# Optimization experiments

Hardware: AMD Instinct MI355X
Metric: run time of the kernel (lower is better)

Reference implementation:

```python
import jax, jax.numpy as jnp
import numpy as np

B, S, I, H = 16, 2048, 1024, 1024


def setup_inputs() -> dict:
    key = jax.random.key(0)
    ks = jax.random.split(key, 12)
    sc = 0.03  # small init so tanh/sigmoid are not saturated
    return {
        "x": jax.random.normal(ks[0], (B, S, I), dtype=jnp.float32),
        "attn_w1": sc * jax.random.normal(ks[1], (H, I), dtype=jnp.float32),
        "attn_b1": sc * jax.random.normal(ks[2], (H,), dtype=jnp.float32),
        "attn_w2": sc * jax.random.normal(ks[3], (1, H), dtype=jnp.float32),
        "attn_b2": sc * jax.random.normal(ks[4], (1,), dtype=jnp.float32),
        "w_ih": sc * jax.random.normal(ks[5], (3 * H, I), dtype=jnp.float32),
        "w_hh": sc * jax.random.normal(ks[6], (3 * H, H), dtype=jnp.float32),
        "b_ih": sc * jax.random.normal(ks[7], (3 * H,), dtype=jnp.float32),
        "b_hh": sc * jax.random.normal(ks[8], (3 * H,), dtype=jnp.float32),
        "fc_w": sc * jax.random.normal(ks[9], (I, H), dtype=jnp.float32),
        "fc_b": sc * jax.random.normal(ks[10], (I,), dtype=jnp.float32),
    }


def reference(x, attn_w1, attn_b1, attn_w2, attn_b2, w_ih, w_hh, b_ih, b_hh, fc_w, fc_b):
    b, s, i = x.shape
    h_dim = w_hh.shape[1]
    # Attention: per-timestep Linear-Tanh-Linear-Softmax, vectorized over time.
    ha = jnp.tanh(jnp.einsum('bsi,hi->bsh', x, attn_w1) + attn_b1)
    scores = jnp.einsum('bsh,oh->bso', ha, attn_w2) + attn_b2  # [B,S,1]
    # torch applies Softmax(dim=1) on [B,1] per timestep -> softmax over size-1 axis
    attn = jax.nn.softmax(scores, axis=2)  # [B,S,1] (identically ones)
    x_w = x * attn
    # GRU (1 layer): precompute input projections over all timesteps.
    gi = jnp.einsum('bsi,gi->bsg', x_w, w_ih) + b_ih  # [B,S,3H]

    def step(h, gi_t):
        gh = h @ w_hh.T + b_hh
        i_r, i_z, i_n = jnp.split(gi_t, 3, axis=-1)
        h_r, h_z, h_n = jnp.split(gh, 3, axis=-1)
        r = jax.nn.sigmoid(i_r + h_r)
        z = jax.nn.sigmoid(i_z + h_z)
        n = jnp.tanh(i_n + r * h_n)
        h_new = (1.0 - z) * n + z * h
        return h_new, h_new

    h0 = jnp.zeros((b, h_dim), dtype=x.dtype)
    h_last, outs = jax.lax.scan(step, h0, jnp.swapaxes(gi, 0, 1))  # outs: [S,B,H]
    rnn_out = jnp.swapaxes(outs, 0, 1)  # [B,S,H]
    output = jnp.einsum('bsh,ih->bsi', rnn_out, fc_w) + fc_b
    hidden = h_last[None]  # [num_layers=1, B, H]
    return (output, hidden, attn)
```

## Files before the change

### kernel.cpp

```cpp
#include <hip/hip_runtime.h>

typedef __attribute__((ext_vector_type(8))) short bh8;
typedef __attribute__((ext_vector_type(4))) float f32x4;

#define BATCH 16
#define SEQ 2048
#define M_ROWS (BATCH * SEQ)
#define KDIM 1024

__device__ __forceinline__ unsigned short f2bf(float f) {
  unsigned u = __float_as_uint(f);
  u = (u + 0x7FFFu + ((u >> 16) & 1u)) >> 16;
  return (unsigned short)u;
}
__device__ __forceinline__ float bf2f(unsigned short h) {
  return __uint_as_float(((unsigned)h) << 16);
}

__device__ __forceinline__ f32x4 mfma_bf16(bh8 a, bh8 b, f32x4 c) {
  return __builtin_amdgcn_mfma_f32_16x16x32_bf16(a, b, c, 0, 0, 0);
}

__device__ __forceinline__ void gl2lds16(const void* g, void* l) {
  __builtin_amdgcn_global_load_lds(
      (const __attribute__((address_space(1))) void*)g,
      (__attribute__((address_space(3))) void*)l, 16, 0, 0);
}

__global__ void cvt_bf16_kernel(const float* __restrict__ in,
                                unsigned short* __restrict__ out, int n4) {
  int i = blockIdx.x * blockDim.x + threadIdx.x;
  if (i >= n4) return;
  float4 v = ((const float4*)in)[i];
  ushort4 o;
  o.x = f2bf(v.x); o.y = f2bf(v.y); o.z = f2bf(v.z); o.w = f2bf(v.w);
  ((ushort4*)out)[i] = o;
}

__global__ void fill_ones_kernel(float* __restrict__ p, int n) {
  int i = blockIdx.x * blockDim.x + threadIdx.x;
  if (i < n) p[i] = 1.0f;
}

template<int MODE>
__global__ __launch_bounds__(256, 2) void gemm_nt(
    const unsigned short* __restrict__ A,
    const unsigned short* __restrict__ Bm,
    void* __restrict__ Cout,
    const float* __restrict__ bias,
    int N)
{
  __shared__ unsigned short As[128 * 32];
  __shared__ unsigned short Bs[128 * 32];
  const int tid = threadIdx.x;
  const int wave = tid >> 6, lane = tid & 63;
  const long tileM = (long)blockIdx.y * 128;
  const long tileN = (long)blockIdx.x * 128;

  const int srow = wave * 16 + (lane >> 2);
  const int scol = (lane & 3) * 8;
  const unsigned short* ga = A + (tileM + srow) * KDIM + scol;
  const unsigned short* gb = Bm + (tileN + srow) * KDIM + scol;
  unsigned short* la = As + wave * 512;
  unsigned short* lb = Bs + wave * 512;

  f32x4 acc[4][4];
  #pragma unroll
  for (int i = 0; i < 4; ++i)
    #pragma unroll
    for (int j = 0; j < 4; ++j)
      acc[i][j] = (f32x4){0.f, 0.f, 0.f, 0.f};

  const int wm = wave >> 1, wn = wave & 1;
  const int q = lane >> 4, mr = lane & 15;

  #pragma unroll 1
  for (int kt = 0; kt < 32; ++kt) {
    const int ko = kt * 32;
    gl2lds16(ga + ko, la);
    gl2lds16(ga + (long)64 * KDIM + ko, la + 2048);
    gl2lds16(gb + ko, lb);
    gl2lds16(gb + (long)64 * KDIM + ko, lb + 2048);
    __syncthreads();

    bh8 af[4], bfv[4];
    #pragma unroll
    for (int t = 0; t < 4; ++t)
      af[t] = *(const bh8*)&As[(wm * 64 + t * 16 + mr) * 32 + q * 8];
    #pragma unroll
    for (int t = 0; t < 4; ++t)
      bfv[t] = *(const bh8*)&Bs[(wn * 64 + t * 16 + mr) * 32 + q * 8];

    #pragma unroll
    for (int mt = 0; mt < 4; ++mt)
      #pragma unroll
      for (int nt = 0; nt < 4; ++nt)
        acc[mt][nt] = mfma_bf16(af[mt], bfv[nt], acc[mt][nt]);
    __syncthreads();
  }

  #pragma unroll
  for (int mt = 0; mt < 4; ++mt) {
    #pragma unroll
    for (int nt = 0; nt < 4; ++nt) {
      long n = tileN + wn * 64 + nt * 16 + mr;
      #pragma unroll
      for (int i = 0; i < 4; ++i) {
        long m = tileM + wm * 64 + mt * 16 + q * 4 + i;
        if constexpr (MODE == 0) {
          ((float*)Cout)[m * N + n] = acc[mt][nt][i] + bias[n];
        } else {
          int b = (int)(m >> 11), s = (int)(m & 2047);
          int g = (int)(n >> 10), wgi = (int)((n >> 4) & 63), dd = (int)(n & 15);
          size_t idx = ((size_t)s * 64 + wgi) * 768 + (size_t)g * 256 + b * 16 + dd;
          ((unsigned short*)Cout)[idx] = f2bf(acc[mt][nt][i]);
        }
      }
    }
  }
}

#define GRU_WGS 64
__global__ __launch_bounds__(256, 1) void gru_kernel(
    const unsigned short* __restrict__ gi,
    const unsigned short* __restrict__ whh,
    const float* __restrict__ b_ih,
    const float* __restrict__ b_hh,
    unsigned* __restrict__ hdw,
    unsigned* __restrict__ flags,
    unsigned short* __restrict__ rnn,
    float* __restrict__ hidden_out)
{
  const int wg = blockIdx.x;
  const int tid = threadIdx.x;
  const int wv = tid >> 6, lane = tid & 63;
  const int D0 = wg * 16;
  const int q = lane >> 4, nn = lane & 15;

  bh8 wf[3][8];
  #pragma unroll
  for (int g = 0; g < 3; ++g)
    #pragma unroll
    for (int kk = 0; kk < 8; ++kk) {
      int k = wv * 256 + kk * 32 + q * 8;
      wf[g][kk] = *(const bh8*)&whh[(size_t)(g * 1024 + D0 + nn) * 1024 + k];
    }

  const int b = tid >> 4, dd = tid & 15, d = D0 + dd;
  const float bir = b_ih[d], biz = b_ih[1024 + d], bin_ = b_ih[2048 + d];
  const float bhr = b_hh[d], bhz = b_hh[1024 + d], bhn = b_hh[2048 + d];
  float hreg = 0.0f;

  __shared__ float red[4][3][16][16];

  const unsigned short* g0 = gi + (size_t)wg * 768 + b * 16 + dd;
  unsigned short pg0 = g0[0], pg1 = g0[256], pg2 = g0[512];

  #pragma unroll 1
  for (int s = 0; s < SEQ; ++s) {
    float gir = bf2f(pg0), giz = bf2f(pg1), gin = bf2f(pg2);

    const unsigned* hrow = hdw + (s & 1) * 8192 + nn * 512 + wv * 128 + q * 4;
    unsigned t[32];
    #pragma unroll
    for (int kk = 0; kk < 8; ++kk)
      #pragma unroll
      for (int j = 0; j < 4; ++j)
        t[kk * 4 + j] = __hip_atomic_load(&hrow[kk * 16 + j], __ATOMIC_RELAXED,
                                          __HIP_MEMORY_SCOPE_AGENT);

    f32x4 acc0 = {0.f,0.f,0.f,0.f}, acc1 = {0.f,0.f,0.f,0.f}, acc2 = {0.f,0.f,0.f,0.f};
    #pragma unroll
    for (int kk = 0; kk < 8; ++kk) {
      union { unsigned w[4]; bh8 v; } u;
      u.w[0] = t[kk*4+0]; u.w[1] = t[kk*4+1]; u.w[2] = t[kk*4+2]; u.w[3] = t[kk*4+3];
      acc0 = mfma_bf16(u.v, wf[0][kk], acc0);
      acc1 = mfma_bf16(u.v, wf[1][kk], acc1);
      acc2 = mfma_bf16(u.v, wf[2][kk], acc2);
    }
    #pragma unroll
    for (int i = 0; i < 4; ++i) {
      red[wv][0][q * 4 + i][nn] = acc0[i];
      red[wv][1][q * 4 + i][nn] = acc1[i];
      red[wv][2][q * 4 + i][nn] = acc2[i];
    }
    __syncthreads();

    float ghr = red[0][0][b][dd] + red[1][0][b][dd] + red[2][0][b][dd] + red[3][0][b][dd];
    float ghz = red[0][1][b][dd] + red[1][1][b][dd] + red[2][1][b][dd] + red[3][1][b][dd];
    float ghn = red[0][2][b][dd] + red[1][2][b][dd] + red[2][2][b][dd] + red[3][2][b][dd];

    float xr = gir + bir + ghr + bhr;
    float xz = giz + biz + ghz + bhz;
    float r = 1.0f / (1.0f + __expf(-xr));
    float z = 1.0f / (1.0f + __expf(-xz));
    float u_ = gin + bin_ + r * (ghn + bhn);
    float e = __expf(-2.0f * fabsf(u_));
    float tt = (1.0f - e) / (1.0f + e);
    float nv = copysignf(tt, u_);
    hreg = (1.0f - z) * nv + z * hreg;

    unsigned short hb = f2bf(hreg);
    unsigned hp = __shfl_xor((unsigned)hb, 1);
    if ((dd & 1) == 0)
      __hip_atomic_store(&hdw[((s + 1) & 1) * 8192 + b * 512 + ((unsigned)d >> 1)],
                         ((unsigned)hb) | (hp << 16),
                         __ATOMIC_RELAXED, __HIP_MEMORY_SCOPE_AGENT);

    rnn[((size_t)b * SEQ + s) * 1024 + d] = hb;
    if (s == SEQ - 1) hidden_out[b * 1024 + d] = hreg;

    __syncthreads();

    if (tid == 0)
      __hip_atomic_store(&flags[wg * 16], (unsigned)(s + 1), __ATOMIC_RELAXED,
                         __HIP_MEMORY_SCOPE_AGENT);

    if (s + 1 < SEQ) {
      const unsigned short* gn = gi + ((size_t)(s + 1) * 64 + wg) * 768 + b * 16 + dd;
      pg0 = gn[0]; pg1 = gn[256]; pg2 = gn[512];
    }

    if (tid < 64) {
      const unsigned tgt = (unsigned)(s + 1);
      unsigned v;
      do {
        v = __hip_atomic_load(&flags[tid * 16], __ATOMIC_RELAXED,
                              __HIP_MEMORY_SCOPE_AGENT);
      } while (__ballot(v >= tgt) != ~0ull);
    }
    __syncthreads();
  }
}

extern "C" void kernel_launch(void* const* d_in, const int* in_sizes, int n_in,
                              void* d_out, int out_size, void* d_ws, size_t ws_size,
                              hipStream_t stream) {
  const float* x    = (const float*)d_in[0];
  const float* w_ih = (const float*)d_in[5];
  const float* w_hh = (const float*)d_in[6];
  const float* b_ih = (const float*)d_in[7];
  const float* b_hh = (const float*)d_in[8];
  const float* fc_w = (const float*)d_in[9];
  const float* fc_b = (const float*)d_in[10];

  float* out        = (float*)d_out;
  float* hidden_out = out + (size_t)M_ROWS * 1024;
  float* attn_out   = hidden_out + 16 * 1024;

  char* ws = (char*)d_ws;
  unsigned short* x_bf   = (unsigned short*)(ws);
  unsigned short* wih_bf = (unsigned short*)(ws + 67108864);
  unsigned short* whh_bf = (unsigned short*)(ws + 73400320);
  unsigned short* fcw_bf = (unsigned short*)(ws + 79691776);
  unsigned short* gi_bf  = (unsigned short*)(ws + 81788928);
  unsigned short* rnn_bf = (unsigned short*)(ws + 283115520);
  unsigned*       hdw    = (unsigned*)(ws + 350224384);
  unsigned*       flags  = (unsigned*)(ws + 350289920);

  hipMemsetAsync(hdw, 0, 65536 + 4096, stream);

  cvt_bf16_kernel<<<32768, 256, 0, stream>>>(x, x_bf, 8388608);
  cvt_bf16_kernel<<<3072, 256, 0, stream>>>(w_ih, wih_bf, 786432);
  cvt_bf16_kernel<<<3072, 256, 0, stream>>>(w_hh, whh_bf, 786432);
  cvt_bf16_kernel<<<1024, 256, 0, stream>>>(fc_w, fcw_bf, 262144);
  fill_ones_kernel<<<128, 256, 0, stream>>>(attn_out, 32768);

  gemm_nt<2><<<dim3(24, 256), 256, 0, stream>>>(x_bf, wih_bf, gi_bf, nullptr, 3072);

  gru_kernel<<<GRU_WGS, 256, 0, stream>>>(gi_bf, whh_bf, b_ih, b_hh, hdw, flags,
                                          rnn_bf, hidden_out);

  gemm_nt<0><<<dim3(8, 256), 256, 0, stream>>>(rnn_bf, fcw_bf, out, fc_b, 1024);
}
```

Before: 11.13 ms.

## Replace flag-based grid barrier with step-tagged hidden-state packets in GRU

Each hidden-state word now carries its timestep tag in the upper 32 bits of a 64-bit atomic store, so consumers poll the data itself instead of waiting on a separate per-workgroup flag barrier. This removes two __syncthreads and the global flag spin per step, and the reduction buffer is double-buffered to avoid a trailing barrier. It doubles the bytes loaded for the hidden state and reuses the start of the workspace (x_bf region, already consumed) for the packet buffer, which is zeroed after the input GEMM.

New measurement: 13.23 ms. 18.8% more time.

```diff
diff --git a/kernel.cpp b/kernel.cpp
--- a/kernel.cpp
+++ b/kernel.cpp
@@ -2,6 +2,7 @@
 
 typedef __attribute__((ext_vector_type(8))) short bh8;
 typedef __attribute__((ext_vector_type(4))) float f32x4;
+typedef unsigned long long u64;
 
 #define BATCH 16
 #define SEQ 2048
@@ -120,14 +121,12 @@
   }
 }
 
-#define GRU_WGS 64
 __global__ __launch_bounds__(256, 1) void gru_kernel(
     const unsigned short* __restrict__ gi,
     const unsigned short* __restrict__ whh,
     const float* __restrict__ b_ih,
     const float* __restrict__ b_hh,
-    unsigned* __restrict__ hdw,
-    unsigned* __restrict__ flags,
+    u64* __restrict__ hq,
     unsigned short* __restrict__ rnn,
     float* __restrict__ hidden_out)
 {
@@ -151,85 +150,85 @@
   const float bhr = b_hh[d], bhz = b_hh[1024 + d], bhn = b_hh[2048 + d];
   float hreg = 0.0f;
 
-  __shared__ float red[4][3][16][16];
+  __shared__ float red[2][4][3][16][16];
 
   const unsigned short* g0 = gi + (size_t)wg * 768 + b * 16 + dd;
   unsigned short pg0 = g0[0], pg1 = g0[256], pg2 = g0[512];
 
   #pragma unroll 1
   for (int s = 0; s < SEQ; ++s) {
+    const int par = s & 1;
+
+    const u64* hrow = hq + par * 8192 + nn * 512 + wv * 128 + q * 4;
+    u64 v[32];
+    for (;;) {
+      #pragma unroll
+      for (int kk = 0; kk < 8; ++kk)
+        #pragma unroll
+        for (int j = 0; j < 4; ++j)
+          v[kk * 4 + j] = __hip_atomic_load(&hrow[kk * 16 + j], __ATOMIC_RELAXED,
+                                            __HIP_MEMORY_SCOPE_AGENT);
+      unsigned mt = 0xffffffffu;
+      #pragma unroll
+      for (int i = 0; i < 32; ++i) {
+        unsigned tg = (unsigned)(v[i] >> 32);
+        mt = tg < mt ? tg : mt;
+      }
+      if (mt >= (unsigned)s) break;
+      __builtin_amdgcn_s_sleep(2);
+    }
+
+    f32x4 acc0 = {0.f,0.f,0.f,0.f}, acc1 = {0.f,0.f,0.f,0.f}, acc2 = {0.f,0.f,0.f,0.f};
+    #pragma unroll
+    for (int kk = 0; kk < 8; ++kk) {
+      union { unsigned w[4]; bh8 f; } u;
+      u.w[0] = (unsigned)v[kk*4+0]; u.w[1] = (unsigned)v[kk*4+1];
+      u.w[2] = (unsigned)v[kk*4+2]; u.w[3] = (unsigned)v[kk*4+3];
+      acc0 = mfma_bf16(u.f, wf[0][kk], acc0);
+      acc1 = mfma_bf16(u.f, wf[1][kk], acc1);
+      acc2 = mfma_bf16(u.f, wf[2][kk], acc2);
+    }
+    #pragma unroll
+    for (int i = 0; i < 4; ++i) {
+      red[par][wv][0][q * 4 + i][nn] = acc0[i];
+      red[par][wv][1][q * 4 + i][nn] = acc1[i];
+      red[par][wv][2][q * 4 + i][nn] = acc2[i];
+    }
+    __syncthreads();
+
+    float ghr = red[par][0][0][b][dd] + red[par][1][0][b][dd]
+              + red[par][2][0][b][dd] + red[par][3][0][b][dd];
+    float ghz = red[par][0][1][b][dd] + red[par][1][1][b][dd]
+              + red[par][2][1][b][dd] + red[par][3][1][b][dd];
+    float ghn = red[par][0][2][b][dd] + red[par][1][2][b][dd]
+              + red[par][2][2][b][dd] + red[par][3][2][b][dd];
+
     float gir = bf2f(pg0), giz = bf2f(pg1), gin = bf2f(pg2);
-
-    const unsigned* hrow = hdw + (s & 1) * 8192 + nn * 512 + wv * 128 + q * 4;
-    unsigned t[32];
-    #pragma unroll
-    for (int kk = 0; kk < 8; ++kk)
-      #pragma unroll
-      for (int j = 0; j < 4; ++j)
-        t[kk * 4 + j] = __hip_atomic_load(&hrow[kk * 16 + j], __ATOMIC_RELAXED,
-                                          __HIP_MEMORY_SCOPE_AGENT);
-
-    f32x4 acc0 = {0.f,0.f,0.f,0.f}, acc1 = {0.f,0.f,0.f,0.f}, acc2 = {0.f,0.f,0.f,0.f};
-    #pragma unroll
-    for (int kk = 0; kk < 8; ++kk) {
-      union { unsigned w[4]; bh8 v; } u;
-      u.w[0] = t[kk*4+0]; u.w[1] = t[kk*4+1]; u.w[2] = t[kk*4+2]; u.w[3] = t[kk*4+3];
-      acc0 = mfma_bf16(u.v, wf[0][kk], acc0);
-      acc1 = mfma_bf16(u.v, wf[1][kk], acc1);
-      acc2 = mfma_bf16(u.v, wf[2][kk], acc2);
-    }
-    #pragma unroll
-    for (int i = 0; i < 4; ++i) {
-      red[wv][0][q * 4 + i][nn] = acc0[i];
-      red[wv][1][q * 4 + i][nn] = acc1[i];
-      red[wv][2][q * 4 + i][nn] = acc2[i];
-    }
-    __syncthreads();
-
-    float ghr = red[0][0][b][dd] + red[1][0][b][dd] + red[2][0][b][dd] + red[3][0][b][dd];
-    float ghz = red[0][1][b][dd] + red[1][1][b][dd] + red[2][1][b][dd] + red[3][1][b][dd];
-    float ghn = red[0][2][b][dd] + red[1][2][b][dd] + red[2][2][b][dd] + red[3][2][b][dd];
-
     float xr = gir + bir + ghr + bhr;
     float xz = giz + biz + ghz + bhz;
     float r = 1.0f / (1.0f + __expf(-xr));
     float z = 1.0f / (1.0f + __expf(-xz));
     float u_ = gin + bin_ + r * (ghn + bhn);
     float e = __expf(-2.0f * fabsf(u_));
-    float tt = (1.0f - e) / (1.0f + e);
-    float nv = copysignf(tt, u_);
+    float tnh = (1.0f - e) / (1.0f + e);
+    float nv = copysignf(tnh, u_);
     hreg = (1.0f - z) * nv + z * hreg;
 
     unsigned short hb = f2bf(hreg);
     unsigned hp = __shfl_xor((unsigned)hb, 1);
-    if ((dd & 1) == 0)
-      __hip_atomic_store(&hdw[((s + 1) & 1) * 8192 + b * 512 + ((unsigned)d >> 1)],
-                         ((unsigned)hb) | (hp << 16),
+    if ((dd & 1) == 0) {
+      u64 pkt = (u64)(((unsigned)hb) | (hp << 16)) | ((u64)(unsigned)(s + 1) << 32);
+      __hip_atomic_store(&hq[(par ^ 1) * 8192 + b * 512 + ((unsigned)d >> 1)], pkt,
                          __ATOMIC_RELAXED, __HIP_MEMORY_SCOPE_AGENT);
+    }
 
     rnn[((size_t)b * SEQ + s) * 1024 + d] = hb;
     if (s == SEQ - 1) hidden_out[b * 1024 + d] = hreg;
-
-    __syncthreads();
-
-    if (tid == 0)
-      __hip_atomic_store(&flags[wg * 16], (unsigned)(s + 1), __ATOMIC_RELAXED,
-                         __HIP_MEMORY_SCOPE_AGENT);
 
     if (s + 1 < SEQ) {
       const unsigned short* gn = gi + ((size_t)(s + 1) * 64 + wg) * 768 + b * 16 + dd;
       pg0 = gn[0]; pg1 = gn[256]; pg2 = gn[512];
     }
-
-    if (tid < 64) {
-      const unsigned tgt = (unsigned)(s + 1);
-      unsigned v;
-      do {
-        v = __hip_atomic_load(&flags[tid * 16], __ATOMIC_RELAXED,
-                              __HIP_MEMORY_SCOPE_AGENT);
-      } while (__ballot(v >= tgt) != ~0ull);
-    }
-    __syncthreads();
   }
 }
 
@@ -255,10 +254,7 @@
   unsigned short* fcw_bf = (unsigned short*)(ws + 79691776);
   unsigned short* gi_bf  = (unsigned short*)(ws + 81788928);
   unsigned short* rnn_bf = (unsigned short*)(ws + 283115520);
-  unsigned*       hdw    = (unsigned*)(ws + 350224384);
-  unsigned*       flags  = (unsigned*)(ws + 350289920);
-
-  hipMemsetAsync(hdw, 0, 65536 + 4096, stream);
+  u64*            hq     = (u64*)(ws);
 
   cvt_bf16_kernel<<<32768, 256, 0, stream>>>(x, x_bf, 8388608);
   cvt_bf16_kernel<<<3072, 256, 0, stream>>>(w_ih, wih_bf, 786432);
@@ -268,8 +264,10 @@
 
   gemm_nt<2><<<dim3(24, 256), 256, 0, stream>>>(x_bf, wih_bf, gi_bf, nullptr, 3072);
 
-  gru_kernel<<<GRU_WGS, 256, 0, stream>>>(gi_bf, whh_bf, b_ih, b_hh, hdw, flags,
-                                          rnn_bf, hidden_out);
+  hipMemsetAsync(hq, 0, 131072, stream);
+
+  gru_kernel<<<64, 256, 0, stream>>>(gi_bf, whh_bf, b_ih, b_hh, hq,
+                                     rnn_bf, hidden_out);
 
   gemm_nt<0><<<dim3(8, 256), 256, 0, stream>>>(rnn_bf, fcw_bf, out, fc_b, 1024);
 }
```
